# Kernel optimization log

Hardware: AMD Instinct MI355X
Metric: run time of the kernel (lower is better)

Reference implementation:

```python
import jax, jax.numpy as jnp
import numpy as np

EPS = 1e-5
HEADS = 4

def _conv(x, w, pad):
    return jax.lax.conv_general_dilated(x, w, (1, 1), [(pad, pad), (pad, pad)],
                                        dimension_numbers=('NCHW', 'OIHW', 'NCHW'))

def _gn(x, g, b, groups=8):
    B, C, H, W = x.shape
    xg = x.reshape(B, groups, C // groups, H, W)
    m = xg.mean((2, 3, 4), keepdims=True)
    v = xg.var((2, 3, 4), keepdims=True)
    xn = ((xg - m) * jax.lax.rsqrt(v + EPS)).reshape(B, C, H, W)
    return xn * g[None, :, None, None] + b[None, :, None, None]

def _bn(x, g, b):  # training-mode BatchNorm2d (batch statistics)
    m = x.mean((0, 2, 3), keepdims=True)
    v = x.var((0, 2, 3), keepdims=True)
    return (x - m) * jax.lax.rsqrt(v + EPS) * g[None, :, None, None] + b[None, :, None, None]

def _resize_ac(x, Ho, Wo):  # bilinear, align_corners=True
    B, C, H, W = x.shape
    if (H, W) == (Ho, Wo):
        return x
    ys = jnp.linspace(0.0, H - 1.0, Ho)
    xs = jnp.linspace(0.0, W - 1.0, Wo)
    y0 = jnp.floor(ys).astype(jnp.int32); y1 = jnp.minimum(y0 + 1, H - 1)
    x0 = jnp.floor(xs).astype(jnp.int32); x1 = jnp.minimum(x0 + 1, W - 1)
    wy = (ys - y0)[None, None, :, None]
    wx = (xs - x0)[None, None, None, :]
    rows = x[:, :, y0, :] * (1.0 - wy) + x[:, :, y1, :] * wy
    return rows[:, :, :, x0] * (1.0 - wx) + rows[:, :, :, x1] * wx

def _idwt_haar(ll, lh, hl, hh):  # single-level inverse haar, zero mode
    B, C, H, W = ll.shape
    x00 = (ll + lh + hl + hh) * 0.5
    x01 = (ll - lh + hl - hh) * 0.5
    x10 = (ll + lh - hl - hh) * 0.5
    x11 = (ll - lh - hl + hh) * 0.5
    r0 = jnp.stack([x00, x01], -1).reshape(B, C, H, 2 * W)
    r1 = jnp.stack([x10, x11], -1).reshape(B, C, H, 2 * W)
    return jnp.stack([r0, r1], 3).reshape(B, C, 2 * H, 2 * W)

def setup_inputs() -> dict:
    key = jax.random.key(0)
    ks = iter(jax.random.split(key, 16))
    def nrm(shape, s=0.05):
        return jax.random.normal(next(ks), shape, jnp.float32) * s
    B, Cin, Cd, H, W = 4, 256, 128, 64, 64
    A = 128  # attention_dim
    return {
        'x': nrm((B, Cin, H, W), 1.0),
        'skip_detail': nrm((B, Cd, H, W), 1.0),
        'skip_structure': nrm((B, Cd, 2 * H, 2 * W), 1.0),
        'skip_global': nrm((B, Cd, H, W), 1.0),
        'W_up': nrm((Cd, Cin, 3, 3)),
        'bn_up_g': jnp.ones(Cd), 'bn_up_b': jnp.zeros(Cd),
        'W_ll': nrm((Cd // 4, Cd, 3, 3)),
        'gn_ll_g': jnp.ones(Cd // 4), 'gn_ll_b': jnp.zeros(Cd // 4),
        'W_high': nrm((3 * Cd // 4, Cd, 3, 3)),
        'gn_high_g': jnp.ones(3 * Cd // 4), 'gn_high_b': jnp.zeros(3 * Cd // 4),
        'w_scale': jnp.float32(3.0),
        'W_adj': nrm((Cd, Cd // 4)),
        'gn_adj_g': jnp.ones(Cd), 'gn_adj_b': jnp.zeros(Cd),
        'Wq': nrm((3, A, Cd)), 'bq': jnp.zeros((3, A)),
        'Wk': nrm((3, A, Cd)), 'bk': jnp.zeros((3, A)),
        'Wv': nrm((3, A, Cd)), 'bv': jnp.zeros((3, A)),
        'W_fuse': nrm((Cd, 3 * A)), 'b_fuse': jnp.zeros(Cd),
        'gn_fuse_g': jnp.ones(Cd), 'gn_fuse_b': jnp.zeros(Cd),
        'gn_out_g': jnp.ones(Cd), 'gn_out_b': jnp.zeros(Cd),
        'W_r1': nrm((Cd, Cd, 3, 3)), 'bn1_g': jnp.ones(Cd), 'bn1_b': jnp.zeros(Cd),
        'W_r2': nrm((Cd, Cd, 3, 3)), 'bn2_g': jnp.ones(Cd), 'bn2_b': jnp.zeros(Cd),
    }

def reference(x, skip_detail, skip_structure, skip_global, W_up, bn_up_g, bn_up_b,
              W_ll, gn_ll_g, gn_ll_b, W_high, gn_high_g, gn_high_b, w_scale,
              W_adj, gn_adj_g, gn_adj_b, Wq, bq, Wk, bk, Wv, bv,
              W_fuse, b_fuse, gn_fuse_g, gn_fuse_b, gn_out_g, gn_out_b,
              W_r1, bn1_g, bn1_b, W_r2, bn2_g, bn2_b):
    B, _, H, W = x.shape
    Ho, Wo = 2 * H, 2 * W
    # --- WaveletReconstructUpsample on skip_detail (spatial matches x) ---
    sd = skip_detail.astype(jnp.float32)
    x_ll = jnp.tanh(_gn(_conv(sd, W_ll, 1), gn_ll_g, gn_ll_b, 8))
    x_hi = jnp.tanh(_gn(_conv(sd, W_high, 1), gn_high_g, gn_high_b, 8))
    scale = jnp.clip(w_scale, 1.0, 5.0)
    x_ll = x_ll * scale
    x_hi = x_hi * scale
    sub = x_ll.shape[1]
    lh, hl, hh = x_hi[:, :sub], x_hi[:, sub:2 * sub], x_hi[:, 2 * sub:]
    rec = _idwt_haar(x_ll, lh, hl, hh)  # (B, sub, Ho, Wo)
    skip_up = jax.nn.relu(_gn(jnp.einsum('oc,bchw->bohw', W_adj, rec), gn_adj_g, gn_adj_b, 8))
    xu = _resize_ac(x, Ho, Wo)
    xu = jax.nn.relu(_bn(_conv(xu, W_up, 1), bn_up_g, bn_up_b))
    merged = xu + skip_up  # (B, Cd, Ho, Wo)
    # --- tri-path multi-scale cross attention (channel attention, d x d) ---
    feats = jnp.stack([skip_up,
                       _resize_ac(skip_structure, Ho, Wo),
                       _resize_ac(skip_global, Ho, Wo)], 0)  # (3,B,C,Ho,Wo)
    A = Wq.shape[1]
    hd = A // HEADS
    N = Ho * Wo
    q = jnp.einsum('poc,bchw->pbohw', Wq, merged) + bq[:, None, :, None, None]
    k = jnp.einsum('poc,pbchw->pbohw', Wk, feats) + bk[:, None, :, None, None]
    v = jnp.einsum('poc,pbchw->pbohw', Wv, feats) + bv[:, None, :, None, None]
    q = q.reshape(3, B, HEADS, hd, N)
    k = k.reshape(3, B, HEADS, hd, N)
    v = v.reshape(3, B, HEADS, hd, N)
    attn = jnp.einsum('pbhdn,pbhen->pbhde', q.astype(jnp.float32), k.astype(jnp.float32))
    attn = jax.nn.softmax(attn / np.float32(np.sqrt(hd)), -1).astype(v.dtype)
    out = jnp.einsum('pbhde,pbhen->pbhdn', attn, v).reshape(3, B, A, Ho, Wo)
    tri = jnp.concatenate([out[0], out[1], out[2]], 1)  # (B, 3A, Ho, Wo)
    fused = jax.nn.silu(_gn(jnp.einsum('oc,bchw->bohw', W_fuse, tri)
                            + b_fuse[None, :, None, None], gn_fuse_g, gn_fuse_b, 8))
    att_out = _gn(merged + fused, gn_out_g, gn_out_b, 8)
    # --- refine conv (dropout is identity in eval / p handled as 0) ---
    r = jax.nn.relu(_bn(_conv(att_out, W_r1, 1), bn1_g, bn1_b))
    r = jax.nn.relu(_bn(_conv(r, W_r2, 1), bn2_g, bn2_b))
    return r
```

## Files before the change

### kernel.cpp

```cpp
#include <hip/hip_runtime.h>
#include <math.h>

#define EPSV 1e-5f

typedef __attribute__((ext_vector_type(8))) short short8;
typedef __attribute__((ext_vector_type(4))) float f32x4;

__device__ inline unsigned short f2bf(float x) {
  unsigned int u = __float_as_uint(x);
  return (unsigned short)((u + 0x7FFFu + ((u >> 16) & 1u)) >> 16);
}
__device__ inline float bf2f(unsigned short v) {
  return __uint_as_float(((unsigned int)v) << 16);
}

__global__ void packall_k(const float* __restrict__ W_up, const float* __restrict__ W_r1,
                          const float* __restrict__ W_r2, const float* __restrict__ W_ll,
                          const float* __restrict__ W_hi, unsigned short* __restrict__ p_up,
                          unsigned short* __restrict__ p_r1, unsigned short* __restrict__ p_r2,
                          unsigned short* __restrict__ p_dt) {
  int idx = blockIdx.x * 256 + threadIdx.x;
  const float* src; unsigned short* dst; int Cin, co_off, local;
  if (idx < 294912)       { src = W_up; dst = p_up; Cin = 256; co_off = 0;  local = idx; }
  else if (idx < 442368)  { src = W_r1; dst = p_r1; Cin = 128; co_off = 0;  local = idx - 294912; }
  else if (idx < 589824)  { src = W_r2; dst = p_r2; Cin = 128; co_off = 0;  local = idx - 442368; }
  else if (idx < 626688)  { src = W_ll; dst = p_dt; Cin = 128; co_off = 0;  local = idx - 589824; }
  else if (idx < 737280)  { src = W_hi; dst = p_dt; Cin = 128; co_off = 32; local = idx - 626688; }
  else return;
  int kk = local % 9;
  int ci = (local / 9) % Cin;
  int co = local / (9 * Cin);
  dst[((long)kk * 128 + co_off + co) * Cin + ci] = f2bf(src[local]);
}

__global__ void t_nhwc_k(const float* __restrict__ in, unsigned short* __restrict__ out,
                         unsigned short* __restrict__ out_nchw, int C, int HW) {
  __shared__ unsigned short lds[64][34];
  int b = blockIdx.z;
  int c0 = blockIdx.y << 5;
  int hw0 = blockIdx.x << 6;
  int t = threadIdx.x;
  int c = t >> 3, j0 = (t & 7) << 3;
  long ibase = ((long)b * C + c0 + c) * HW + hw0 + j0;
  const float* p = in + ibase;
  int4 nv; unsigned short* ns = (unsigned short*)&nv;
#pragma unroll
  for (int j = 0; j < 8; j++) {
    unsigned short v = f2bf(p[j]);
    lds[j0 + j][c] = v;
    ns[j] = v;
  }
  if (out_nchw) *(int4*)(out_nchw + ibase) = nv;
  __syncthreads();
  int hw = t >> 2, k = (t & 3) << 3;
  unsigned short* q = out + ((long)(b * HW + hw0 + hw)) * C + c0 + k;
  int4 val;
  unsigned short* vs = (unsigned short*)&val;
#pragma unroll
  for (int i = 0; i < 8; i++) vs[i] = lds[hw][k + i];
  *(int4*)q = val;
}

__global__ void gnout_nhwc_k(const float* __restrict__ in, const float* __restrict__ sums,
                             const float* __restrict__ gamma, const float* __restrict__ beta,
                             unsigned short* __restrict__ out) {
  __shared__ unsigned short lds[64][34];
  int b = blockIdx.z;
  int c0 = blockIdx.y << 5;
  int hw0 = blockIdx.x << 6;
  int t = threadIdx.x;
  int c = t >> 3, j0 = (t & 7) << 3;
  int ch = c0 + c;
  int sidx = b * 8 + (ch >> 4);
  const float ic = 1.f / 262144.f;
  float m = sums[2 * sidx] * ic;
  float r = rsqrtf(fmaxf(sums[2 * sidx + 1] * ic - m * m, 0.f) + EPSV);
  float ga = gamma[ch] * r, be = beta[ch] - m * r * gamma[ch];
  const float* p = in + (((long)(b * 128 + ch)) << 14) + hw0 + j0;
#pragma unroll
  for (int j = 0; j < 8; j++) lds[j0 + j][c] = f2bf(p[j] * ga + be);
  __syncthreads();
  int hw = t >> 2, k = (t & 3) << 3;
  unsigned short* q = out + ((long)(b * 16384 + hw0 + hw)) * 128 + c0 + k;
  int4 val;
  unsigned short* vs = (unsigned short*)&val;
#pragma unroll
  for (int i = 0; i < 8; i++) vs[i] = lds[hw][k + i];
  *(int4*)q = val;
}

__global__ void bnrelu_nhwc_k(const float* __restrict__ in, const float* __restrict__ sums,
                              const float* __restrict__ gamma, const float* __restrict__ beta,
                              unsigned short* __restrict__ out) {
  __shared__ unsigned short lds[64][34];
  int b = blockIdx.z;
  int c0 = blockIdx.y << 5;
  int hw0 = blockIdx.x << 6;
  int t = threadIdx.x;
  int c = t >> 3, j0 = (t & 7) << 3;
  int ch = c0 + c;
  const float ic = 1.f / 65536.f;
  float m = sums[2 * ch] * ic;
  float r = rsqrtf(fmaxf(sums[2 * ch + 1] * ic - m * m, 0.f) + EPSV);
  float ga = gamma[ch] * r, be = beta[ch] - m * r * gamma[ch];
  const float* p = in + (((long)(b * 128 + ch)) << 14) + hw0 + j0;
#pragma unroll
  for (int j = 0; j < 8; j++) lds[j0 + j][c] = f2bf(fmaxf(p[j] * ga + be, 0.f));
  __syncthreads();
  int hw = t >> 2, k = (t & 3) << 3;
  unsigned short* q = out + ((long)(b * 16384 + hw0 + hw)) * 128 + c0 + k;
  int4 val;
  unsigned short* vs = (unsigned short*)&val;
#pragma unroll
  for (int i = 0; i < 8; i++) vs[i] = lds[hw][k + i];
  *(int4*)q = val;
}

__global__ __launch_bounds__(256) void resize_t_k(const float* __restrict__ in,
                                                  unsigned short* __restrict__ out,
                                                  int C, float s) {
  __shared__ float rows[2][32][68];
  int ho = blockIdx.x, cb = blockIdx.y, b = blockIdx.z;
  int t = threadIdx.x;
  float ys = ho * s;
  int y0 = (int)ys; float wy = ys - y0;
  int y1 = min(y0 + 1, 63);
  for (int i = t; i < 1024; i += 256) {
    int r = i >> 9, c = (i >> 4) & 31, seg = i & 15;
    const float* p = in + (((long)(b * C + cb * 32 + c)) << 12) + ((r ? y1 : y0) << 6) + (seg << 2);
    *(float4*)&rows[r][c][seg << 2] = *(const float4*)p;
  }
  __syncthreads();
  int cs = t & 3;
#pragma unroll
  for (int half = 0; half < 2; half++) {
    int wo = (t >> 2) + half * 64;
    float xs = wo * s;
    int x0 = (int)xs; float wx = xs - x0;
    int x1 = min(x0 + 1, 63);
    int4 val; unsigned short* vs = (unsigned short*)&val;
#pragma unroll
    for (int j = 0; j < 8; j++) {
      int c = cs * 8 + j;
      float v00 = rows[0][c][x0], v01 = rows[0][c][x1];
      float v10 = rows[1][c][x0], v11 = rows[1][c][x1];
      float r0 = v00 + (v01 - v00) * wx;
      float r1 = v10 + (v11 - v10) * wx;
      vs[j] = f2bf(r0 + (r1 - r0) * wy);
    }
    *(int4*)(out + ((long)((b * 128 + ho) * 128 + wo)) * C + cb * 32 + cs * 8) = val;
  }
}

__global__ void resize_nchwbf_k(const float* __restrict__ in, unsigned short* __restrict__ out,
                                float s) {
  long idx = (long)blockIdx.x * 256 + threadIdx.x;
  int seg = (int)(idx & 15); long t2 = idx >> 4;
  int ho = (int)(t2 & 127); t2 >>= 7;
  int c = (int)(t2 & 127); int b = (int)(t2 >> 7);
  float ys = ho * s;
  int y0 = (int)ys; float wy = ys - y0;
  int y1 = min(y0 + 1, 63);
  const float* p = in + (((long)(b * 128 + c)) << 12);
  int4 val; unsigned short* vs = (unsigned short*)&val;
#pragma unroll
  for (int j = 0; j < 8; j++) {
    int wo = seg * 8 + j;
    float xs = wo * s;
    int x0 = (int)xs; float wx = xs - x0;
    int x1 = min(x0 + 1, 63);
    float v00 = p[(y0 << 6) + x0], v01 = p[(y0 << 6) + x1];
    float v10 = p[(y1 << 6) + x0], v11 = p[(y1 << 6) + x1];
    float r0 = v00 + (v01 - v00) * wx;
    float r1 = v10 + (v11 - v10) * wx;
    vs[j] = f2bf(r0 + (r1 - r0) * wy);
  }
  *(int4*)(out + (((long)(b * 128 + c)) << 14) + (ho << 7) + seg * 8) = val;
}

template <int W_, int CIN, int COB, int FC, int FN>
__global__ __launch_bounds__(256) void conv2_k(
    const unsigned short* __restrict__ xin, const unsigned short* __restrict__ wpk,
    float* __restrict__ out, int H) {
  constexpr int CP = 40;
  __shared__ unsigned short wbuf[3 * COB * CP];
  __shared__ unsigned short rbuf[(W_ + 2) * CP];
  int h = blockIdx.x, b = blockIdx.y, cb = blockIdx.z;
  int t = threadIdx.x;
  int wid = t >> 6, lane = t & 63;
  int co0 = (wid >> 1) * (FC * 16);
  int n0 = (wid & 1) * (FN * 16);
  int lm = lane & 15, lk = lane >> 4;
  f32x4 acc[FC][FN];
#pragma unroll
  for (int i = 0; i < FC; i++)
#pragma unroll
    for (int j = 0; j < FN; j++) acc[i][j] = (f32x4){0.f, 0.f, 0.f, 0.f};

  constexpr int WEL = 3 * COB * 32 / 8;
  constexpr int REL = (W_ + 2) * 32 / 8;

  for (int c0 = 0; c0 < CIN; c0 += 32) {
    for (int ky = 0; ky < 3; ky++) {
      int hr = h + ky - 1;
      __syncthreads();
      for (int i = t; i < WEL + REL; i += 256) {
        if (i < WEL) {
          int e = i * 8;
          int kx = e / (COB * 32);
          int rem = e - kx * (COB * 32);
          int co = rem >> 5, ci = rem & 31;
          const unsigned short* g =
              wpk + ((long)((ky * 3 + kx) * 128 + cb * COB + co)) * CIN + c0 + ci;
          *(int4*)&wbuf[(kx * COB + co) * CP + ci] = *(const int4*)g;
        } else {
          int e = (i - WEL) * 8;
          int col = e >> 5, ci = e & 31;
          int gc = col - 1;
          int4 v = {0, 0, 0, 0};
          if (hr >= 0 && hr < H && gc >= 0 && gc < W_)
            v = *(const int4*)(xin + ((long)((b * H + hr) * W_ + gc)) * CIN + c0 + ci);
          *(int4*)&rbuf[col * CP + ci] = v;
        }
      }
      __syncthreads();
#pragma unroll
      for (int kx = 0; kx < 3; kx++) {
        short8 afr[FC], bfr[FN];
#pragma unroll
        for (int i = 0; i < FC; i++)
          afr[i] = *(const short8*)&wbuf[(kx * COB + co0 + i * 16 + lm) * CP + lk * 8];
#pragma unroll
        for (int j = 0; j < FN; j++)
          bfr[j] = *(const short8*)&rbuf[(n0 + j * 16 + lm + kx) * CP + lk * 8];
#pragma unroll
        for (int i = 0; i < FC; i++)
#pragma unroll
          for (int j = 0; j < FN; j++)
            acc[i][j] = __builtin_amdgcn_mfma_f32_16x16x32_bf16(afr[i], bfr[j], acc[i][j], 0, 0, 0);
      }
    }
  }
#pragma unroll
  for (int i = 0; i < FC; i++) {
#pragma unroll
    for (int r = 0; r < 4; r++) {
      int col = cb * COB + co0 + i * 16 + lk * 4 + r;
      long obase = (((long)(b * 128 + col)) * H + h) * W_;
#pragma unroll
      for (int j = 0; j < FN; j++)
        out[obase + n0 + j * 16 + lm] = acc[i][j][r];
    }
  }
}

__global__ void gn_sums_k(const float* __restrict__ x, float* __restrict__ sums,
                          int Ctot, int coff, int cpg, int HW, int goff) {
  int bg = blockIdx.x; int b = bg >> 3, g = bg & 7;
  const float* p = x + ((long)b * Ctot + coff + (long)g * cpg) * HW;
  long len = (long)cpg * HW;
  long chunk = len / gridDim.y;
  long s = (long)blockIdx.y * chunk, e = s + chunk;
  float s0 = 0.f, s1 = 0.f;
  for (long i = s + threadIdx.x; i < e; i += 256) {
    float v = p[i]; s0 += v; s1 += v * v;
  }
  __shared__ float r0[256], r1[256];
  int t = threadIdx.x;
  r0[t] = s0; r1[t] = s1;
  __syncthreads();
  for (int off = 128; off > 0; off >>= 1) {
    if (t < off) { r0[t] += r0[t + off]; r1[t] += r1[t + off]; }
    __syncthreads();
  }
  if (t == 0) {
    int gi = b * 16 + goff + g;
    atomicAdd(&sums[2 * gi], r0[0]);
    atomicAdd(&sums[2 * gi + 1], r1[0]);
  }
}

__global__ void bn_sums_k(const float* __restrict__ x, float* __restrict__ sums, int C) {
  int c = blockIdx.x;
  long total = 4L << 14;
  long chunk = total / gridDim.y;
  long s = (long)blockIdx.y * chunk, e = s + chunk;
  float s0 = 0.f, s1 = 0.f;
  for (long i = s + threadIdx.x; i < e; i += 256) {
    int b = (int)(i >> 14); int hw = (int)(i & 16383);
    float v = x[(((long)b * C + c) << 14) + hw];
    s0 += v; s1 += v * v;
  }
  __shared__ float r0[256], r1[256];
  int t = threadIdx.x;
  r0[t] = s0; r1[t] = s1;
  __syncthreads();
  for (int off = 128; off > 0; off >>= 1) {
    if (t < off) { r0[t] += r0[t + off]; r1[t] += r1[t + off]; }
    __syncthreads();
  }
  if (t == 0) { atomicAdd(&sums[2 * c], r0[0]); atomicAdd(&sums[2 * c + 1], r1[0]); }
}

__global__ void idwt_k(const float* __restrict__ det, const float* __restrict__ sd,
                       const float* __restrict__ gll, const float* __restrict__ bll,
                       const float* __restrict__ ghi, const float* __restrict__ bhi,
                       const float* __restrict__ wsc, float* __restrict__ rec) {
  long idx = ((long)blockIdx.x << 8) + threadIdx.x;
  if (idx >= (long)4 * 32 * 64 * 64) return;
  int j = (int)(idx & 63); long t = idx >> 6;
  int i = (int)(t & 63); t >>= 6;
  int c = (int)(t & 31); int b = (int)(t >> 5);
  float s = wsc[0]; s = fminf(fmaxf(s, 1.f), 5.f);
  const float icll = 1.f / 16384.f, ichi = 1.f / 49152.f;
  const float* dp = det + ((long)b << 19);
  long sp = ((long)i << 6) + j;
  int gi = b * 16 + (c >> 2);
  float m = sd[2 * gi] * icll;
  float r = rsqrtf(fmaxf(sd[2 * gi + 1] * icll - m * m, 0.f) + EPSV);
  float ll = tanhf((dp[((long)c << 12) + sp] - m) * r * gll[c] + bll[c]) * s;
  int hc = c; gi = b * 16 + 8 + hc / 12;
  m = sd[2 * gi] * ichi; r = rsqrtf(fmaxf(sd[2 * gi + 1] * ichi - m * m, 0.f) + EPSV);
  float lh = tanhf((dp[((long)(32 + hc) << 12) + sp] - m) * r * ghi[hc] + bhi[hc]) * s;
  hc = 32 + c; gi = b * 16 + 8 + hc / 12;
  m = sd[2 * gi] * ichi; r = rsqrtf(fmaxf(sd[2 * gi + 1] * ichi - m * m, 0.f) + EPSV);
  float hl = tanhf((dp[((long)(32 + hc) << 12) + sp] - m) * r * ghi[hc] + bhi[hc]) * s;
  hc = 64 + c; gi = b * 16 + 8 + hc / 12;
  m = sd[2 * gi] * ichi; r = rsqrtf(fmaxf(sd[2 * gi + 1] * ichi - m * m, 0.f) + EPSV);
  float hh = tanhf((dp[((long)(32 + hc) << 12) + sp] - m) * r * ghi[hc] + bhi[hc]) * s;
  float x00 = (ll + lh + hl + hh) * 0.5f;
  float x01 = (ll - lh + hl - hh) * 0.5f;
  float x10 = (ll + lh - hl - hh) * 0.5f;
  float x11 = (ll - lh - hl + hh) * 0.5f;
  float* rp = rec + (((long)b * 32 + c) << 14) + ((long)i << 8) + (j << 1);
  rp[0] = x00; rp[1] = x01; rp[128] = x10; rp[129] = x11;
}

__global__ __launch_bounds__(256) void adj_k(const float* __restrict__ rec,
                                             const float* __restrict__ Wadj,
                                             float* __restrict__ out,
                                             float* __restrict__ gsums) {
  __shared__ float ls[32][256];
  int n0 = blockIdx.x << 8;
  int o0 = blockIdx.y << 4;
  int b = blockIdx.z;
  int t = threadIdx.x;
  for (int idx = t; idx < 32 * 256; idx += 256) {
    int c = idx >> 8, n = idx & 255;
    ls[c][n] = rec[(((long)b * 32 + c) << 14) + n0 + n];
  }
  __syncthreads();
  float acc[16];
#pragma unroll
  for (int i = 0; i < 16; i++) acc[i] = 0.f;
  for (int c = 0; c < 32; c++) {
    float v = ls[c][t];
#pragma unroll
    for (int i = 0; i < 16; i++) acc[i] += v * Wadj[(o0 + i) * 32 + c];
  }
  float s0 = 0.f, s1 = 0.f;
#pragma unroll
  for (int i = 0; i < 16; i++) {
    out[(((long)b * 128 + o0 + i) << 14) + n0 + t] = acc[i];
    s0 += acc[i]; s1 += acc[i] * acc[i];
  }
  __syncthreads();
  float* red = (float*)ls;
  red[t] = s0; red[256 + t] = s1;
  __syncthreads();
  for (int off = 128; off > 0; off >>= 1) {
    if (t < off) { red[t] += red[t + off]; red[256 + t] += red[256 + t + off]; }
    __syncthreads();
  }
  if (t == 0) {
    int gi = b * 8 + (o0 >> 4);
    atomicAdd(&gsums[2 * gi], red[0]);
    atomicAdd(&gsums[2 * gi + 1], red[256]);
  }
}

__global__ void gn_relu_k(float* __restrict__ x, const float* __restrict__ sums,
                          const float* __restrict__ gamma, const float* __restrict__ beta) {
  long i0 = ((long)blockIdx.x * 256 + threadIdx.x) * 8;
  int ch = (int)((i0 >> 14) & 127);
  int b = (int)(i0 >> 21);
  int sidx = b * 8 + (ch >> 4);
  const float ic = 1.f / 262144.f;
  float m = sums[2 * sidx] * ic;
  float r = rsqrtf(fmaxf(sums[2 * sidx + 1] * ic - m * m, 0.f) + EPSV);
  float ga = gamma[ch] * r, be = beta[ch] - m * r * gamma[ch];
#pragma unroll
  for (int j = 0; j < 8; j++) {
    float v = fmaxf(x[i0 + j] * ga + be, 0.f);
    x[i0 + j] = v;
  }
}

__global__ void bn_apply8_k(float* __restrict__ x, const float* __restrict__ sums,
                            const float* __restrict__ gamma, const float* __restrict__ beta,
                            const float* __restrict__ add, unsigned short* __restrict__ obf) {
  long i0 = ((long)blockIdx.x * 256 + threadIdx.x) * 8;
  int ch = (int)((i0 >> 14) & 127);
  const float ic = 1.f / 65536.f;
  float m = sums[2 * ch] * ic;
  float r = rsqrtf(fmaxf(sums[2 * ch + 1] * ic - m * m, 0.f) + EPSV);
  float ga = gamma[ch] * r, be = beta[ch] - m * r * gamma[ch];
  int4 ov; unsigned short* os = (unsigned short*)&ov;
#pragma unroll
  for (int j = 0; j < 8; j++) {
    float v = fmaxf(x[i0 + j] * ga + be, 0.f);
    if (add) v += add[i0 + j];
    x[i0 + j] = v;
    os[j] = f2bf(v);
  }
  if (obf) *(int4*)(obf + i0) = ov;
}

__global__ void gn_silu_add_k(float* __restrict__ x, const float* __restrict__ sums,
                              const float* __restrict__ gamma, const float* __restrict__ beta,
                              const float* __restrict__ add, float* __restrict__ osums) {
  long i0 = ((long)blockIdx.x * 256 + threadIdx.x) * 8;
  int ch = (int)((i0 >> 14) & 127);
  int b = (int)(i0 >> 21);
  int sidx = b * 8 + (ch >> 4);
  const float ic = 1.f / 262144.f;
  float m = sums[2 * sidx] * ic;
  float r = rsqrtf(fmaxf(sums[2 * sidx + 1] * ic - m * m, 0.f) + EPSV);
  float ga = gamma[ch] * r, be = beta[ch] - m * r * gamma[ch];
  float s0 = 0.f, s1 = 0.f;
#pragma unroll
  for (int j = 0; j < 8; j++) {
    float v = x[i0 + j] * ga + be;
    v = v / (1.f + expf(-v));
    v += add[i0 + j];
    x[i0 + j] = v;
    s0 += v; s1 += v * v;
  }
  __shared__ float r0[256], r1[256];
  int t = threadIdx.x;
  r0[t] = s0; r1[t] = s1;
  __syncthreads();
  for (int off = 128; off > 0; off >>= 1) {
    if (t < off) { r0[t] += r0[t + off]; r1[t] += r1[t + off]; }
    __syncthreads();
  }
  if (t == 0) {
    atomicAdd(&osums[2 * sidx], r0[0]);
    atomicAdd(&osums[2 * sidx + 1], r1[0]);
  }
}

__global__ void colsum4_k(const unsigned short* __restrict__ m, const unsigned short* __restrict__ f0,
                          const unsigned short* __restrict__ f1, const unsigned short* __restrict__ f2,
                          float* __restrict__ S) {
  int bc = blockIdx.x, which = blockIdx.y;
  const unsigned short* p = (which == 0 ? m : which == 1 ? f0 : which == 2 ? f1 : f2) + ((long)bc << 14);
  float a = 0.f;
  for (int i = threadIdx.x; i < 2048; i += 256) {
    int4 v = *(const int4*)(p + i * 8);
    unsigned short* vs = (unsigned short*)&v;
#pragma unroll
    for (int j = 0; j < 8; j++) a += bf2f(vs[j]);
  }
  __shared__ float red[256];
  red[threadIdx.x] = a;
  __syncthreads();
  for (int off = 128; off > 0; off >>= 1) {
    if (threadIdx.x < off) red[threadIdx.x] += red[threadIdx.x + off];
    __syncthreads();
  }
  if (threadIdx.x == 0) S[which * 512 + bc] = red[0];
}

__global__ __launch_bounds__(256) void gram_mfma_k(
    const unsigned short* __restrict__ mbf, const unsigned short* __restrict__ f0,
    const unsigned short* __restrict__ f1, const unsigned short* __restrict__ f2,
    float* __restrict__ Gpart) {
  constexpr int CP = 40;
  __shared__ unsigned short As[128 * CP], Bs[128 * CP];
  int nc = blockIdx.x, p = blockIdx.y, b = blockIdx.z;
  const unsigned short* fp = (p == 0 ? f0 : p == 1 ? f1 : f2);
  const unsigned short* ma = mbf + ((long)b << 21);
  const unsigned short* fa = fp + ((long)b << 21);
  int t = threadIdx.x;
  int wid = t >> 6, lane = t & 63;
  int c0 = (wid >> 1) << 6;
  int cp0 = (wid & 1) << 6;
  int lm = lane & 15, lk = lane >> 4;
  f32x4 acc[4][4];
#pragma unroll
  for (int i = 0; i < 4; i++)
#pragma unroll
    for (int j = 0; j < 4; j++) acc[i][j] = (f32x4){0.f, 0.f, 0.f, 0.f};
  for (int ks = 0; ks < 16; ks++) {
    int n = (nc << 9) + (ks << 5);
    __syncthreads();
#pragma unroll
    for (int i = 0; i < 2; i++) {
      int idx = t + (i << 8);
      int row = idx >> 2, q = idx & 3;
      *(int4*)&As[row * CP + q * 8] = *(const int4*)(ma + ((long)row << 14) + n + q * 8);
      *(int4*)&Bs[row * CP + q * 8] = *(const int4*)(fa + ((long)row << 14) + n + q * 8);
    }
    __syncthreads();
    short8 af[4], bfr[4];
#pragma unroll
    for (int i = 0; i < 4; i++) af[i] = *(const short8*)&As[(c0 + i * 16 + lm) * CP + lk * 8];
#pragma unroll
    for (int j = 0; j < 4; j++) bfr[j] = *(const short8*)&Bs[(cp0 + j * 16 + lm) * CP + lk * 8];
#pragma unroll
    for (int i = 0; i < 4; i++)
#pragma unroll
      for (int j = 0; j < 4; j++)
        acc[i][j] = __builtin_amdgcn_mfma_f32_16x16x32_bf16(af[i], bfr[j], acc[i][j], 0, 0, 0);
  }
  float* Gp = Gpart + (((long)(nc * 12 + p * 4 + b)) << 14);
#pragma unroll
  for (int i = 0; i < 4; i++)
#pragma unroll
    for (int j = 0; j < 4; j++) {
      int cp = cp0 + j * 16 + lm;
#pragma unroll
      for (int r = 0; r < 4; r++) {
        int c = c0 + i * 16 + lk * 4 + r;
        Gp[c * 128 + cp] = acc[i][j][r];
      }
    }
}

__global__ void gred_k(const float* __restrict__ Gpart, float* __restrict__ G) {
  int cell = blockIdx.x * 256 + threadIdx.x;
  int pb = cell >> 14, rem = cell & 16383;
  float a = 0.f;
  for (int nc = 0; nc < 32; nc++) a += Gpart[(((long)(nc * 12 + pb)) << 14) + rem];
  G[cell] = a;
}

__global__ __launch_bounds__(256) void attn_k(const float* __restrict__ G,
                                              const float* __restrict__ Sall,
                                              const float* __restrict__ Wq,
                                              const float* __restrict__ bq,
                                              const float* __restrict__ Wk,
                                              const float* __restrict__ bk,
                                              float* __restrict__ attn) {
  int h = blockIdx.x, b = blockIdx.y, p = blockIdx.z;
  __shared__ float T[32][129];
  __shared__ float QS2[32], KS1[32];
  __shared__ float L[32][33];
  const float* S2 = Sall;
  const float* S1 = Sall + 512;
  const float* Gpb = G + ((long)(p * 4 + b) << 14);
  const float* Wqp = Wq + p * 16384;
  const float* Wkp = Wk + p * 16384;
  int t = threadIdx.x;
  if (t < 32) {
    float a = 0.f;
    for (int c = 0; c < 128; c++) a += Wqp[(h * 32 + t) * 128 + c] * S2[b * 128 + c];
    QS2[t] = a;
  } else if (t < 64) {
    int e = t - 32;
    float a = 0.f;
    for (int c = 0; c < 128; c++) a += Wkp[(h * 32 + e) * 128 + c] * S1[(p * 4 + b) * 128 + c];
    KS1[e] = a;
  }
  __syncthreads();
  for (int ii = t; ii < 4096; ii += 256) {
    int d = ii >> 7, cp = ii & 127;
    float a = 0.f;
    for (int c = 0; c < 128; c++) a += Wqp[(h * 32 + d) * 128 + c] * Gpb[c * 128 + cp];
    T[d][cp] = a;
  }
  __syncthreads();
  const float scale = 0.17677669529663687f;
  for (int ii = t; ii < 1024; ii += 256) {
    int d = ii >> 5, e = ii & 31;
    float a = 0.f;
    for (int cp = 0; cp < 128; cp++) a += T[d][cp] * Wkp[(h * 32 + e) * 128 + cp];
    float bqv = bq[p * 128 + h * 32 + d], bkv = bk[p * 128 + h * 32 + e];
    a += bqv * KS1[e] + bkv * QS2[d] + 16384.f * bqv * bkv;
    L[d][e] = a * scale;
  }
  __syncthreads();
  if (t < 32) {
    float mx = -1e30f;
    for (int e = 0; e < 32; e++) mx = fmaxf(mx, L[t][e]);
    float sum = 0.f;
    for (int e = 0; e < 32; e++) { float ev = expf(L[t][e] - mx); L[t][e] = ev; sum += ev; }
    float inv = 1.f / sum;
    float* ap = attn + ((((long)(p * 4 + b)) * 4 + h) * 32 + t) * 32;
    for (int e = 0; e < 32; e++) ap[e] = L[t][e] * inv;
  }
}

__global__ void m_k(const float* __restrict__ Wf, const float* __restrict__ attn,
                    const float* __restrict__ bv, float* __restrict__ M,
                    float* __restrict__ cbias) {
  int o = blockIdx.x, b = blockIdx.y, p = blockIdx.z;
  int ap = threadIdx.x;
  int h = ap >> 5;
  const float* at = attn + (((long)(p * 4 + b)) * 4 + h) * 1024;
  const float* wrow = Wf + o * 384 + p * 128 + h * 32;
  int e = ap & 31;
  float acc = 0.f;
  for (int d = 0; d < 32; d++) acc += wrow[d] * at[d * 32 + e];
  M[(((long)(p * 4 + b)) * 128 + o) * 128 + ap] = acc;
  __shared__ float red[128];
  red[ap] = acc * bv[p * 128 + ap];
  __syncthreads();
  for (int off = 64; off > 0; off >>= 1) {
    if (ap < off) red[ap] += red[ap + off];
    __syncthreads();
  }
  if (ap == 0) atomicAdd(&cbias[b * 128 + o], red[0]);
}

__global__ void weff_k(const float* __restrict__ M, const float* __restrict__ Wv,
                       unsigned short* __restrict__ Weff) {
  int o = blockIdx.x, b = blockIdx.y, p = blockIdx.z, c = threadIdx.x;
  const float* mrow = M + (((long)(p * 4 + b)) * 128 + o) * 128;
  const float* wv = Wv + p * 16384;
  float acc = 0.f;
  for (int a = 0; a < 128; a++) acc += mrow[a] * wv[a * 128 + c];
  Weff[((long)(b * 128 + o)) * 384 + p * 128 + c] = f2bf(acc);
}

__global__ __launch_bounds__(256) void fuse_mfma_k(
    const unsigned short* __restrict__ Wef, const unsigned short* __restrict__ f0t,
    const unsigned short* __restrict__ f1t, const unsigned short* __restrict__ f2t,
    const float* __restrict__ bf_, const float* __restrict__ cbias,
    float* __restrict__ out, float* __restrict__ gsums) {
  constexpr int CP = 40;
  __shared__ unsigned short As[64 * CP], Bs[128 * CP];
  __shared__ float sred[8];
  int nc = blockIdx.x, ob = blockIdx.y, b = blockIdx.z;
  int t = threadIdx.x;
  int wid = t >> 6, lane = t & 63;
  int o0 = (wid >> 1) * 32;
  int n0 = (wid & 1) * 64;
  int lm = lane & 15, lk = lane >> 4;
  if (t < 8) sred[t] = 0.f;
  f32x4 acc[2][4];
#pragma unroll
  for (int i = 0; i < 2; i++)
#pragma unroll
    for (int j = 0; j < 4; j++) acc[i][j] = (f32x4){0.f, 0.f, 0.f, 0.f};
  for (int kp = 0; kp < 12; kp++) {
    int k0 = kp << 5;
    int p = k0 >> 7, cc0 = k0 & 127;
    const unsigned short* ft = (p == 0 ? f0t : p == 1 ? f1t : f2t);
    __syncthreads();
    for (int i = t; i < 768; i += 256) {
      if (i < 256) {
        int row = i >> 2, q = i & 3;
        *(int4*)&As[row * CP + q * 8] =
            *(const int4*)(Wef + ((long)(b * 128 + ob * 64 + row)) * 384 + k0 + q * 8);
      } else {
        int j2 = i - 256;
        int n = j2 >> 2, q = j2 & 3;
        *(int4*)&Bs[n * CP + q * 8] =
            *(const int4*)(ft + ((long)(b * 16384 + nc * 128 + n)) * 128 + cc0 + q * 8);
      }
    }
    __syncthreads();
    short8 af[2], bfr[4];
#pragma unroll
    for (int i = 0; i < 2; i++) af[i] = *(const short8*)&As[(o0 + i * 16 + lm) * CP + lk * 8];
#pragma unroll
    for (int j = 0; j < 4; j++) bfr[j] = *(const short8*)&Bs[(n0 + j * 16 + lm) * CP + lk * 8];
#pragma unroll
    for (int i = 0; i < 2; i++)
#pragma unroll
      for (int j = 0; j < 4; j++)
        acc[i][j] = __builtin_amdgcn_mfma_f32_16x16x32_bf16(af[i], bfr[j], acc[i][j], 0, 0, 0);
  }
#pragma unroll
  for (int i = 0; i < 2; i++) {
    float s0 = 0.f, s1 = 0.f;
#pragma unroll
    for (int r = 0; r < 4; r++) {
      int o = ob * 64 + o0 + i * 16 + lk * 4 + r;
      float bias = bf_[o] + cbias[b * 128 + o];
#pragma unroll
      for (int j = 0; j < 4; j++) {
        int n = (nc << 7) + n0 + j * 16 + lm;
        float v = acc[i][j][r] + bias;
        out[(((long)(b * 128 + o)) << 14) + n] = v;
        s0 += v; s1 += v * v;
      }
    }
#pragma unroll
    for (int off = 1; off < 64; off <<= 1) {
      s0 += __shfl_xor(s0, off, 64);
      s1 += __shfl_xor(s1, off, 64);
    }
    if (lane == 0) {
      int gl = (o0 >> 4) + i;
      atomicAdd(&sred[2 * gl], s0);
      atomicAdd(&sred[2 * gl + 1], s1);
    }
  }
  __syncthreads();
  if (t < 8) {
    int g = b * 8 + ob * 4 + (t >> 1);
    atomicAdd(&gsums[2 * g + (t & 1)], sred[t]);
  }
}

extern "C" void kernel_launch(void* const* d_in, const int* in_sizes, int n_in,
                              void* d_out, int out_size, void* d_ws, size_t ws_size,
                              hipStream_t stream) {
  const float* x      = (const float*)d_in[0];
  const float* sdet   = (const float*)d_in[1];
  const float* sstru  = (const float*)d_in[2];
  const float* sglob  = (const float*)d_in[3];
  const float* W_up   = (const float*)d_in[4];
  const float* bnug   = (const float*)d_in[5];
  const float* bnub   = (const float*)d_in[6];
  const float* W_ll   = (const float*)d_in[7];
  const float* gllg   = (const float*)d_in[8];
  const float* gllb   = (const float*)d_in[9];
  const float* W_hi   = (const float*)d_in[10];
  const float* ghig   = (const float*)d_in[11];
  const float* ghib   = (const float*)d_in[12];
  const float* wsc    = (const float*)d_in[13];
  const float* W_adj  = (const float*)d_in[14];
  const float* gadjg  = (const float*)d_in[15];
  const float* gadjb  = (const float*)d_in[16];
  const float* Wq     = (const float*)d_in[17];
  const float* bq     = (const float*)d_in[18];
  const float* Wk     = (const float*)d_in[19];
  const float* bk     = (const float*)d_in[20];
  const float* Wv     = (const float*)d_in[21];
  const float* bv     = (const float*)d_in[22];
  const float* W_fu   = (const float*)d_in[23];
  const float* b_fu   = (const float*)d_in[24];
  const float* gfug   = (const float*)d_in[25];
  const float* gfub   = (const float*)d_in[26];
  const float* goug   = (const float*)d_in[27];
  const float* goub   = (const float*)d_in[28];
  const float* W_r1   = (const float*)d_in[29];
  const float* bn1g   = (const float*)d_in[30];
  const float* bn1b   = (const float*)d_in[31];
  const float* W_r2   = (const float*)d_in[32];
  const float* bn2g   = (const float*)d_in[33];
  const float* bn2b   = (const float*)d_in[34];
  float* out = (float*)d_out;

  float* ws = (float*)d_ws;
  size_t off = 0;
  auto alloc = [&](size_t n) { float* p = ws + off; off += n; return p; };
  float* bufA = alloc(8388608);
  float* det  = bufA;
  float* rec  = bufA + 2097152;
  float* Gpart = bufA;
  float* bufB = alloc(8388608);
  float* bufC = alloc(8388608);
  unsigned short* f1t = (unsigned short*)bufC;
  unsigned short* f2t = (unsigned short*)bufC + 8388608;
  unsigned short* xbf = (unsigned short*)alloc(8388608);
  unsigned short* f0t = (unsigned short*)alloc(4194304);
  unsigned short* mbf = (unsigned short*)alloc(4194304);
  unsigned short* f0  = (unsigned short*)alloc(4194304);
  unsigned short* f1  = (unsigned short*)alloc(4194304);
  unsigned short* f2  = (unsigned short*)alloc(4194304);
  float* Gm   = alloc(196608);
  unsigned short* wpk_up = (unsigned short*)alloc(147456);
  unsigned short* wpk_r1 = (unsigned short*)alloc(73728);
  unsigned short* wpk_r2 = (unsigned short*)alloc(73728);
  unsigned short* wpk_dt = (unsigned short*)alloc(36864);
  unsigned short* wefb   = (unsigned short*)alloc(98304);
  float* Sall = alloc(2048);
  float* attb = alloc(49152);
  float* Mb   = alloc(196608);
  float* zr = alloc(1600);
  float* cb      = zr;
  float* s_det   = zr + 512;
  float* s_adj   = zr + 640;
  float* s_bnup  = zr + 704;
  float* s_fuse  = zr + 960;
  float* s_gnout = zr + 1024;
  float* s_bn1   = zr + 1088;
  float* s_bn2   = zr + 1344;

  const float s63 = 63.f / 127.f;

  hipMemsetAsync(zr, 0, 1600 * sizeof(float), stream);
  packall_k<<<2880, 256, 0, stream>>>(W_up, W_r1, W_r2, W_ll, W_hi,
                                      wpk_up, wpk_r1, wpk_r2, wpk_dt);

  t_nhwc_k<<<dim3(64, 4, 4), 256, 0, stream>>>(sdet, xbf, nullptr, 128, 4096);
  conv2_k<64, 128, 32, 1, 2><<<dim3(64, 4, 4), 256, 0, stream>>>(xbf, wpk_dt, det, 64);
  gn_sums_k<<<dim3(32, 4), 256, 0, stream>>>(det, s_det, 128, 0, 4, 4096, 0);
  gn_sums_k<<<dim3(32, 8), 256, 0, stream>>>(det, s_det, 128, 32, 12, 4096, 8);
  idwt_k<<<2048, 256, 0, stream>>>(det, s_det, gllg, gllb, ghig, ghib, wsc, rec);

  adj_k<<<dim3(64, 8, 4), 256, 0, stream>>>(rec, W_adj, bufC, s_adj);
  gn_relu_k<<<4096, 256, 0, stream>>>(bufC, s_adj, gadjg, gadjb);

  resize_t_k<<<dim3(128, 8, 4), 256, 0, stream>>>(x, xbf, 256, s63);
  conv2_k<128, 256, 128, 4, 4><<<dim3(128, 4), 256, 0, stream>>>(xbf, wpk_up, bufB, 128);
  bn_sums_k<<<dim3(128, 16), 256, 0, stream>>>(bufB, s_bnup, 128);
  bn_apply8_k<<<4096, 256, 0, stream>>>(bufB, s_bnup, bnug, bnub, bufC, mbf);

  t_nhwc_k<<<dim3(256, 4, 4), 256, 0, stream>>>(bufC, f0t, f0, 128, 16384);
  t_nhwc_k<<<dim3(256, 4, 4), 256, 0, stream>>>(sstru, f1t, f1, 128, 16384);
  resize_nchwbf_k<<<4096, 256, 0, stream>>>(sglob, f2, s63);
  resize_t_k<<<dim3(128, 4, 4), 256, 0, stream>>>(sglob, f2t, 128, s63);

  colsum4_k<<<dim3(512, 4), 256, 0, stream>>>(mbf, f0, f1, f2, Sall);
  gram_mfma_k<<<dim3(32, 3, 4), 256, 0, stream>>>(mbf, f0, f1, f2, Gpart);
  gred_k<<<768, 256, 0, stream>>>(Gpart, Gm);
  attn_k<<<dim3(4, 4, 3), 256, 0, stream>>>(Gm, Sall, Wq, bq, Wk, bk, attb);

  m_k<<<dim3(128, 4, 3), 128, 0, stream>>>(W_fu, attb, bv, Mb, cb);
  weff_k<<<dim3(128, 4, 3), 128, 0, stream>>>(Mb, Wv, wefb);
  fuse_mfma_k<<<dim3(128, 2, 4), 256, 0, stream>>>(wefb, f0t, f1t, f2t, b_fu, cb, bufA, s_fuse);

  gn_silu_add_k<<<4096, 256, 0, stream>>>(bufA, s_fuse, gfug, gfub, bufB, s_gnout);
  gnout_nhwc_k<<<dim3(256, 4, 4), 256, 0, stream>>>(bufA, s_gnout, goug, goub, xbf);

  conv2_k<128, 128, 128, 4, 4><<<dim3(128, 4), 256, 0, stream>>>(xbf, wpk_r1, bufB, 128);
  bn_sums_k<<<dim3(128, 16), 256, 0, stream>>>(bufB, s_bn1, 128);
  bnrelu_nhwc_k<<<dim3(256, 4, 4), 256, 0, stream>>>(bufB, s_bn1, bn1g, bn1b, xbf);

  conv2_k<128, 128, 128, 4, 4><<<dim3(128, 4), 256, 0, stream>>>(xbf, wpk_r2, out, 128);
  bn_sums_k<<<dim3(128, 16), 256, 0, stream>>>(out, s_bn2, 128);
  bn_apply8_k<<<4096, 256, 0, stream>>>(out, s_bn2, bn2g, bn2b, nullptr, nullptr);
}
```

Baseline: 909.1 us.

## Add conv3_k: register-held weights, 3-row LDS halo, split output channels across blocks

Adds a new 3x3 conv kernel that loads all nine taps' weight fragments straight from global memory into registers for each 32-channel input slice. It stages a 3-row input halo in LDS, so the weights no longer pass through shared memory. The grid gains a z dimension that splits the 128 output channels into two 64-channel halves, doubling block count for better occupancy. The trade-off is higher register pressure (9*FC short8 fragments) and each input tile being loaded twice, once per channel half. It replaces conv2_k for the upsample conv and both refine convs.

```diff
diff --git a/kernel.cpp b/kernel.cpp
--- a/kernel.cpp
+++ b/kernel.cpp
@@ -246,6 +246,77 @@
 #pragma unroll
     for (int r = 0; r < 4; r++) {
       int col = cb * COB + co0 + i * 16 + lk * 4 + r;
+      long obase = (((long)(b * 128 + col)) * H + h) * W_;
+#pragma unroll
+      for (int j = 0; j < FN; j++)
+        out[obase + n0 + j * 16 + lm] = acc[i][j][r];
+    }
+  }
+}
+
+template <int W_, int CIN, int COB, int FC, int FN>
+__global__ __launch_bounds__(256) void conv3_k(
+    const unsigned short* __restrict__ xin, const unsigned short* __restrict__ wpk,
+    float* __restrict__ out, int H) {
+  constexpr int CP = 40;
+  __shared__ unsigned short rbuf[3 * (W_ + 2) * CP];
+  int h = blockIdx.x, b = blockIdx.y, cb = blockIdx.z;
+  int t = threadIdx.x;
+  int wid = t >> 6, lane = t & 63;
+  int co0 = cb * COB + (wid >> 1) * (FC * 16);
+  int n0 = (wid & 1) * (FN * 16);
+  int lm = lane & 15, lk = lane >> 4;
+  f32x4 acc[FC][FN];
+#pragma unroll
+  for (int i = 0; i < FC; i++)
+#pragma unroll
+    for (int j = 0; j < FN; j++) acc[i][j] = (f32x4){0.f, 0.f, 0.f, 0.f};
+
+  constexpr int RW = W_ + 2;
+  constexpr int REL = 3 * RW * 32 / 8;
+
+  for (int c0 = 0; c0 < CIN; c0 += 32) {
+    short8 afr[9][FC];
+#pragma unroll
+    for (int kk = 0; kk < 9; kk++)
+#pragma unroll
+      for (int i = 0; i < FC; i++)
+        afr[kk][i] = *(const short8*)(wpk +
+            ((long)(kk * 128 + co0 + i * 16 + lm)) * CIN + c0 + lk * 8);
+    __syncthreads();
+    for (int i = t; i < REL; i += 256) {
+      int r = i / (RW * 4);
+      int rem = i - r * (RW * 4);
+      int col = rem >> 2, q = rem & 3;
+      int hr = h + r - 1, gc = col - 1;
+      int4 v = {0, 0, 0, 0};
+      if (hr >= 0 && hr < H && gc >= 0 && gc < W_)
+        v = *(const int4*)(xin + ((long)((b * H + hr) * W_ + gc)) * CIN + c0 + q * 8);
+      *(int4*)&rbuf[(r * RW + col) * CP + q * 8] = v;
+    }
+    __syncthreads();
+#pragma unroll
+    for (int ky = 0; ky < 3; ky++) {
+#pragma unroll
+      for (int kx = 0; kx < 3; kx++) {
+        short8 bfr[FN];
+#pragma unroll
+        for (int j = 0; j < FN; j++)
+          bfr[j] = *(const short8*)&rbuf[(ky * RW + n0 + j * 16 + lm + kx) * CP + lk * 8];
+#pragma unroll
+        for (int i = 0; i < FC; i++)
+#pragma unroll
+          for (int j = 0; j < FN; j++)
+            acc[i][j] = __builtin_amdgcn_mfma_f32_16x16x32_bf16(afr[ky * 3 + kx][i], bfr[j],
+                                                                acc[i][j], 0, 0, 0);
+      }
+    }
+  }
+#pragma unroll
+  for (int i = 0; i < FC; i++) {
+#pragma unroll
+    for (int r = 0; r < 4; r++) {
+      int col = co0 + i * 16 + lk * 4 + r;
       long obase = (((long)(b * 128 + col)) * H + h) * W_;
 #pragma unroll
       for (int j = 0; j < FN; j++)
@@ -798,7 +869,7 @@
   gn_relu_k<<<4096, 256, 0, stream>>>(bufC, s_adj, gadjg, gadjb);
 
   resize_t_k<<<dim3(128, 8, 4), 256, 0, stream>>>(x, xbf, 256, s63);
-  conv2_k<128, 256, 128, 4, 4><<<dim3(128, 4), 256, 0, stream>>>(xbf, wpk_up, bufB, 128);
+  conv3_k<128, 256, 64, 2, 4><<<dim3(128, 4, 2), 256, 0, stream>>>(xbf, wpk_up, bufB, 128);
   bn_sums_k<<<dim3(128, 16), 256, 0, stream>>>(bufB, s_bnup, 128);
   bn_apply8_k<<<4096, 256, 0, stream>>>(bufB, s_bnup, bnug, bnub, bufC, mbf);
 
@@ -819,11 +890,11 @@
   gn_silu_add_k<<<4096, 256, 0, stream>>>(bufA, s_fuse, gfug, gfub, bufB, s_gnout);
   gnout_nhwc_k<<<dim3(256, 4, 4), 256, 0, stream>>>(bufA, s_gnout, goug, goub, xbf);
 
-  conv2_k<128, 128, 128, 4, 4><<<dim3(128, 4), 256, 0, stream>>>(xbf, wpk_r1, bufB, 128);
+  conv3_k<128, 128, 64, 2, 4><<<dim3(128, 4, 2), 256, 0, stream>>>(xbf, wpk_r1, bufB, 128);
   bn_sums_k<<<dim3(128, 16), 256, 0, stream>>>(bufB, s_bn1, 128);
   bnrelu_nhwc_k<<<dim3(256, 4, 4), 256, 0, stream>>>(bufB, s_bn1, bn1g, bn1b, xbf);
 
-  conv2_k<128, 128, 128, 4, 4><<<dim3(128, 4), 256, 0, stream>>>(xbf, wpk_r2, out, 128);
+  conv3_k<128, 128, 64, 2, 4><<<dim3(128, 4, 2), 256, 0, stream>>>(xbf, wpk_r2, out, 128);
   bn_sums_k<<<dim3(128, 16), 256, 0, stream>>>(out, s_bn2, 128);
   bn_apply8_k<<<4096, 256, 0, stream>>>(out, s_bn2, bn2g, bn2b, nullptr, nullptr);
 }
```

Measured after the change: 943.6 us. 3.8% more time.
